# Performance work log

Hardware: AMD Instinct MI355X
Metric: run time of the kernel (lower is better)

Reference implementation:

```python
import jax, jax.numpy as jnp
import numpy as np

NUM_HEADS = 16
HEAD_DIM = 64
HIDDEN = NUM_HEADS * HEAD_DIM
LN_EPS = 1e-6


def setup_inputs() -> dict:
    key = jax.random.key(0)
    ks = jax.random.split(key, 5)
    B, T, H = 2, 2048, HIDDEN
    s = 1.0 / np.sqrt(H)
    return {
        "h": jax.random.normal(ks[0], (B, T, H), jnp.float32),
        "Wq": jax.random.normal(ks[1], (H, H), jnp.float32) * s,
        "bq": jnp.zeros((H,), jnp.float32),
        "Wk": jax.random.normal(ks[2], (H, H), jnp.float32) * s,
        "bk": jnp.zeros((H,), jnp.float32),
        "Wv": jax.random.normal(ks[3], (H, H), jnp.float32) * s,
        "bv": jnp.zeros((H,), jnp.float32),
        "Wo": jax.random.normal(ks[4], (H, H), jnp.float32) * s,
        "bo": jnp.zeros((H,), jnp.float32),
        "gamma": jnp.ones((H,), jnp.float32),
        "beta": jnp.zeros((H,), jnp.float32),
    }


def _split_heads(x):
    B, T, H = x.shape
    return x.reshape(B, T, NUM_HEADS, HEAD_DIM).transpose(0, 2, 1, 3)  # [B,h,T,d]


def reference(h, Wq, bq, Wk, bk, Wv, bv, Wo, bo, gamma, beta):
    # QKV projections (nn.Linear: x @ W^T + b)
    Q = _split_heads(h @ Wq.T + bq)
    K = _split_heads(h @ Wk.T + bk)
    V = _split_heads(h @ Wv.T + bv)
    scale = HEAD_DIM ** -0.5
    scores = jnp.einsum("bhqd,bhkd->bhqk", Q, K) * scale  # [B,h,T,T]
    attn = jax.nn.softmax(scores, axis=-1)
    ctx = jnp.einsum("bhqk,bhkd->bhqd", attn, V)          # [B,h,T,d]
    B, _, T, _ = ctx.shape
    ctx = ctx.transpose(0, 2, 1, 3).reshape(B, T, HIDDEN)
    out = ctx @ Wo.T + bo + h  # dropout is identity at eval
    # LayerNorm(eps=1e-6)
    mu = out.mean(-1, keepdims=True)
    var = jnp.mean((out - mu) ** 2, -1, keepdims=True)
    return (out - mu) * jax.lax.rsqrt(var + LN_EPS) * gamma + beta
```

## Files before the change

### kernel.cpp

```cpp
#include <hip/hip_runtime.h>
#include <hip/hip_bf16.h>

#define NH   16
#define HD   64
#define HID  1024
#define TSEQ 2048
#define BATCH 2
#define KSCALE 0.18033688011112042f

typedef __attribute__((ext_vector_type(4))) float f32x4;
typedef __attribute__((ext_vector_type(8))) short s16x8;
typedef __attribute__((ext_vector_type(4))) short s16x4;
typedef __attribute__((ext_vector_type(8))) _Float16 f16x8;
typedef __attribute__((ext_vector_type(4))) _Float16 f16x4;
typedef __attribute__((ext_vector_type(2))) _Float16 f16x2;

__device__ __forceinline__ unsigned short f2bf(float f) {
  union { float f; unsigned int u; } v; v.f = f;
  unsigned int r = v.u + 0x7fffu + ((v.u >> 16) & 1u);
  return (unsigned short)(r >> 16);
}
__device__ __forceinline__ float bf2f(unsigned short b) {
  union { unsigned int u; float f; } v; v.u = ((unsigned int)b) << 16; return v.f;
}

__device__ __forceinline__ void gll16(const void* g, void* l) {
  __builtin_amdgcn_global_load_lds(
      (const __attribute__((address_space(1))) unsigned int*)g,
      (__attribute__((address_space(3))) unsigned int*)l, 16, 0, 0);
}

#define WAITBAR(N)                                                      \
  do {                                                                  \
    __builtin_amdgcn_sched_barrier(0);                                  \
    asm volatile("s_waitcnt vmcnt(" #N ")\n\ts_barrier" ::: "memory");  \
  } while (0)

__global__ __launch_bounds__(256) void cast_all_k(
    const float* __restrict__ h,
    const float* __restrict__ w0, const float* __restrict__ w1,
    const float* __restrict__ w2, const float* __restrict__ w3,
    unsigned short* __restrict__ hb, unsigned short* __restrict__ wbase) {
  int i = blockIdx.x * 256 + threadIdx.x;
  const float* src; unsigned short* dst; int idx; float sc = 1.f;
  if (i < 1048576) { src = h; dst = hb; idx = i; }
  else {
    int idx4 = i - 1048576;
    int w = idx4 >> 18;
    idx = idx4 & 262143;
    src = (w == 0) ? w0 : (w == 1) ? w1 : (w == 2) ? w2 : w3;
    dst = wbase + (size_t)(idx4 - idx) * 4;
    if (w == 1) sc = KSCALE;
  }
  float4 v = ((const float4*)src)[idx];
  ushort4 o;
  o.x = f2bf(v.x * sc); o.y = f2bf(v.y * sc); o.z = f2bf(v.z * sc); o.w = f2bf(v.w * sc);
  ((ushort4*)dst)[idx] = o;
}

__global__ __launch_bounds__(256) void gemm_qkv(
    const unsigned short* __restrict__ hb,
    const unsigned short* __restrict__ wcat,
    const float* __restrict__ bq, const float* __restrict__ bk, const float* __restrict__ bv,
    unsigned short* __restrict__ qo, unsigned short* __restrict__ ko,
    unsigned short* __restrict__ vto) {
  __shared__ unsigned short Ash[4][128 * 32];
  __shared__ unsigned short Bsh[4][192 * 32];
  const int tid = threadIdx.x, lane = tid & 63, wave = tid >> 6;
  const int l15 = lane & 15, quad = lane >> 4;
  const int wr = wave >> 1, wc = wave & 1;
  const int bn = blockIdx.x * 192, bm = blockIdx.y * 128;
  const char* Ab = (const char*)(hb + (size_t)bm * HID);
  const char* Bb = (const char*)(wcat + (size_t)bn * HID);
  const int off = tid * 16;
  const int r0 = off >> 6, c0 = off & 63;
  const size_t ga0 = (size_t)r0 * (HID * 2) + c0;
  const size_t ga1 = ga0 + (size_t)64  * (HID * 2);
  const size_t gb2 = ga0 + (size_t)128 * (HID * 2);
  const int lb0 = wave * 512;
  const int lb1 = 2048 + wave * 512;
  const int lb2 = 4096 + wave * 512;

  f32x4 acc[4][6];
#pragma unroll
  for (int i = 0; i < 4; ++i)
#pragma unroll
    for (int j = 0; j < 6; ++j) acc[i][j] = f32x4{0.f, 0.f, 0.f, 0.f};

  auto stage = [&](int bufi, int k0) {
    const size_t kb = (size_t)k0 * 2;
    gll16(Ab + ga0 + kb, &Ash[bufi][lb0]);
    gll16(Ab + ga1 + kb, &Ash[bufi][lb1]);
    gll16(Bb + ga0 + kb, &Bsh[bufi][lb0]);
    gll16(Bb + ga1 + kb, &Bsh[bufi][lb1]);
    gll16(Bb + gb2 + kb, &Bsh[bufi][lb2]);
  };
  auto compute = [&](int bufi) {
    s16x8 af[4], bfr[6];
#pragma unroll
    for (int i = 0; i < 4; ++i)
      af[i] = *(const s16x8*)(&Ash[bufi][(wr * 64 + i * 16 + l15) * 32 + quad * 8]);
#pragma unroll
    for (int j = 0; j < 6; ++j)
      bfr[j] = *(const s16x8*)(&Bsh[bufi][(wc * 96 + j * 16 + l15) * 32 + quad * 8]);
#pragma unroll
    for (int i = 0; i < 4; ++i)
#pragma unroll
      for (int j = 0; j < 6; ++j)
        acc[i][j] = __builtin_amdgcn_mfma_f32_16x16x32_bf16(af[i], bfr[j], acc[i][j], 0, 0, 0);
  };

  stage(0, 0);
  stage(1, 32);
  stage(2, 64);
  int cur = 0, pf = 3;
  const int NT = HID / 32;
  for (int t = 0; t < NT - 3; ++t) {
    WAITBAR(10);
    stage(pf, (t + 3) * 32);
    compute(cur);
    cur = (cur + 1) & 3;
    pf  = (pf + 1) & 3;
  }
  WAITBAR(10); compute(cur); cur = (cur + 1) & 3;
  WAITBAR(5);  compute(cur); cur = (cur + 1) & 3;
  WAITBAR(0);  compute(cur);

  const int rbase = bm + wr * 64;
#pragma unroll
  for (int j = 0; j < 6; ++j) {
    const int cg  = bn + wc * 96 + j * 16;
    const int mat = cg >> 10;
    const int coln = (cg & 1023) + l15;
    const int head = coln >> 6, d = coln & 63;
    if (mat == 2) {
      const float bb = bv[coln];
#pragma unroll
      for (int i = 0; i < 4; ++i) {
        const int row0 = rbase + i * 16 + quad * 4;
        const int bI = row0 >> 11, t0 = row0 & 2047;
        unsigned short o[4];
#pragma unroll
        for (int r = 0; r < 4; ++r) {
          _Float16 hv = (_Float16)(acc[i][j][r] + bb);
          o[r] = __builtin_bit_cast(unsigned short, hv);
        }
        *(s16x4*)(vto + ((size_t)((bI * NH + head) * HD + d)) * TSEQ + t0) = *(const s16x4*)o;
      }
    } else {
      unsigned short* dst = (mat == 0) ? qo : ko;
      const float bb = (mat == 0) ? bq[coln] : bk[coln] * KSCALE;
#pragma unroll
      for (int i = 0; i < 4; ++i) {
#pragma unroll
        for (int r = 0; r < 4; ++r) {
          const int row = rbase + i * 16 + quad * 4 + r;
          const int bI = row >> 11, t = row & 2047;
          dst[(((size_t)(bI * NH + head) * TSEQ) + t) * HD + d] = f2bf(acc[i][j][r] + bb);
        }
      }
    }
  }
}

__global__ __launch_bounds__(256) void gemm_out(
    const unsigned short* __restrict__ ctx, const unsigned short* __restrict__ wo,
    const float* __restrict__ bo, const float* __restrict__ hres,
    float* __restrict__ outf) {
  __shared__ unsigned short Ash[5][128 * 32];
  __shared__ unsigned short Bsh[5][64 * 32];
  const int tid = threadIdx.x, lane = tid & 63, wave = tid >> 6;
  const int l15 = lane & 15, quad = lane >> 4;
  const int wr = wave >> 1, wc = wave & 1;
  const int bn = blockIdx.x * 64, bm = blockIdx.y * 128;
  const char* Ab = (const char*)(ctx + (size_t)bm * HID);
  const char* Bb = (const char*)(wo + (size_t)bn * HID);
  const int off = tid * 16;
  const int r0 = off >> 6, c0 = off & 63;
  const size_t ga0 = (size_t)r0 * (HID * 2) + c0;
  const size_t ga1 = ga0 + (size_t)64 * (HID * 2);
  const int lb0 = wave * 512, lb1 = 2048 + wave * 512;

  f32x4 acc[4][2];
#pragma unroll
  for (int i = 0; i < 4; ++i)
#pragma unroll
    for (int j = 0; j < 2; ++j) acc[i][j] = f32x4{0.f, 0.f, 0.f, 0.f};

  auto stage = [&](int bufi, int k0) {
    const size_t kb = (size_t)k0 * 2;
    gll16(Ab + ga0 + kb, &Ash[bufi][lb0]);
    gll16(Ab + ga1 + kb, &Ash[bufi][lb1]);
    gll16(Bb + ga0 + kb, &Bsh[bufi][lb0]);
  };
  auto compute = [&](int bufi) {
    s16x8 af[4], bfr[2];
#pragma unroll
    for (int i = 0; i < 4; ++i)
      af[i] = *(const s16x8*)(&Ash[bufi][(wr * 64 + i * 16 + l15) * 32 + quad * 8]);
#pragma unroll
    for (int j = 0; j < 2; ++j)
      bfr[j] = *(const s16x8*)(&Bsh[bufi][(wc * 32 + j * 16 + l15) * 32 + quad * 8]);
#pragma unroll
    for (int i = 0; i < 4; ++i)
#pragma unroll
      for (int j = 0; j < 2; ++j)
        acc[i][j] = __builtin_amdgcn_mfma_f32_16x16x32_bf16(af[i], bfr[j], acc[i][j], 0, 0, 0);
  };

  stage(0, 0);
  stage(1, 32);
  stage(2, 64);
  stage(3, 96);
  int cur = 0, pf = 4;
  const int NT = HID / 32;
  for (int t = 0; t < NT - 4; ++t) {
    WAITBAR(9);
    stage(pf, (t + 4) * 32);
    compute(cur);
    cur = (cur == 4) ? 0 : cur + 1;
    pf  = (pf  == 4) ? 0 : pf + 1;
  }
  WAITBAR(9); compute(cur); cur = (cur == 4) ? 0 : cur + 1;
  WAITBAR(6); compute(cur); cur = (cur == 4) ? 0 : cur + 1;
  WAITBAR(3); compute(cur); cur = (cur == 4) ? 0 : cur + 1;
  WAITBAR(0); compute(cur);

#pragma unroll
  for (int j = 0; j < 2; ++j) {
    const int col = bn + wc * 32 + j * 16 + l15;
    const float bb = bo[col];
#pragma unroll
    for (int i = 0; i < 4; ++i) {
#pragma unroll
      for (int r = 0; r < 4; ++r) {
        const int row = bm + wr * 64 + i * 16 + quad * 4 + r;
        const size_t o = (size_t)row * HID + col;
        outf[o] = acc[i][j][r] + bb + hres[o];
      }
    }
  }
}

__global__ __launch_bounds__(256, 2) void attn_k(
    const unsigned short* __restrict__ qb, const unsigned short* __restrict__ kb,
    const unsigned short* __restrict__ vt, unsigned short* __restrict__ ctx,
    unsigned short* __restrict__ Opart, float* __restrict__ rsumP,
    int lsplit, int ntiles) {
  __shared__ unsigned short Ksh[3][64 * 72];
  __shared__ unsigned short Vsh[3][64 * 72];

  const int tid = threadIdx.x, lane = tid & 63, wave = tid >> 6;
  const int l15 = lane & 15, quad = lane >> 4;
  const int z = blockIdx.z;
  const int b = z >> lsplit;
  const int part = z & ((1 << lsplit) - 1);
  const int h = blockIdx.y, qt = blockIdx.x;
  const size_t ho = ((size_t)(b * NH + h)) * TSEQ * HD;
  const unsigned short* Qh = qb + ho;
  const unsigned short* Kh = kb + ho;
  const unsigned short* Vh = vt + ho;
  const int q0 = qt * 128 + wave * 32;
  const int kt0 = part * ntiles;

  s16x8 qf[2][2];
#pragma unroll
  for (int s = 0; s < 2; ++s)
#pragma unroll
    for (int ks = 0; ks < 2; ++ks)
      qf[s][ks] = *(const s16x8*)(Qh + (size_t)(q0 + s * 16 + l15) * HD + ks * 32 + quad * 8);

  f32x4 accO[4][2];
  f32x4 accR[2];
#pragma unroll
  for (int n2 = 0; n2 < 4; ++n2)
#pragma unroll
    for (int s = 0; s < 2; ++s) accO[n2][s] = f32x4{0.f, 0.f, 0.f, 0.f};
  accR[0] = accR[1] = f32x4{0.f, 0.f, 0.f, 0.f};
  const f16x8 vones = {(_Float16)1.f, (_Float16)1.f, (_Float16)1.f, (_Float16)1.f,
                       (_Float16)1.f, (_Float16)1.f, (_Float16)1.f, (_Float16)1.f};

  const int sr = tid >> 3, sc = (tid & 7) * 8;
  const int c = tid & 7;
  const int vwb = (c >> 2) * 32 + (c & 1) * 16 + ((c & 3) >> 1) * 4;
  s16x8 kreg[2], vreg[2];

  auto ldregs = [&](int kt) {
    const int k0n = (kt0 + kt) * 64;
#pragma unroll
    for (int hf = 0; hf < 2; ++hf) {
      kreg[hf] = *(const s16x8*)(Kh + (size_t)(k0n + sr + hf * 32) * HD + sc);
      vreg[hf] = *(const s16x8*)(Vh + (size_t)(sr + hf * 32) * TSEQ + k0n + sc);
    }
  };
  auto wlds = [&](int bi) {
#pragma unroll
    for (int hf = 0; hf < 2; ++hf) {
      *(s16x8*)(Ksh[bi] + (sr + hf * 32) * 72 + sc) = kreg[hf];
      const s16x4* vh = (const s16x4*)&vreg[hf];
      *(s16x4*)(Vsh[bi] + (sr + hf * 32) * 72 + vwb)     = vh[0];
      *(s16x4*)(Vsh[bi] + (sr + hf * 32) * 72 + vwb + 8) = vh[1];
    }
  };

  f32x4 accS[2][4];
  f16x4 pP[2][4];

  auto qkt = [&](int bi) {
#pragma unroll
    for (int s = 0; s < 2; ++s)
#pragma unroll
      for (int n = 0; n < 4; ++n) accS[s][n] = f32x4{0.f, 0.f, 0.f, 0.f};
    __builtin_amdgcn_s_setprio(1);
#pragma unroll
    for (int ks = 0; ks < 2; ++ks) {
#pragma unroll
      for (int n = 0; n < 4; ++n) {
        s16x8 kf = *(const s16x8*)(Ksh[bi] + (n * 16 + l15) * 72 + ks * 32 + quad * 8);
#pragma unroll
        for (int s = 0; s < 2; ++s)
          accS[s][n] = __builtin_amdgcn_mfma_f32_16x16x32_bf16(kf, qf[s][ks], accS[s][n], 0, 0, 0);
      }
    }
    __builtin_amdgcn_s_setprio(0);
  };
  auto expp = [&]() {
#pragma unroll
    for (int s = 0; s < 2; ++s)
#pragma unroll
      for (int n = 0; n < 4; ++n) {
        float e0 = __builtin_amdgcn_exp2f(accS[s][n][0]);
        float e1 = __builtin_amdgcn_exp2f(accS[s][n][1]);
        float e2 = __builtin_amdgcn_exp2f(accS[s][n][2]);
        float e3 = __builtin_amdgcn_exp2f(accS[s][n][3]);
        f16x2 lo = __builtin_bit_cast(f16x2, __builtin_amdgcn_cvt_pkrtz(e0, e1));
        f16x2 hi = __builtin_bit_cast(f16x2, __builtin_amdgcn_cvt_pkrtz(e2, e3));
        pP[s][n] = f16x4{lo[0], lo[1], hi[0], hi[1]};
      }
  };
  auto pv = [&](int bi) {
    __builtin_amdgcn_s_setprio(1);
#pragma unroll
    for (int kk = 0; kk < 2; ++kk) {
      union { f16x4 h[2]; f16x8 v8; } u0, u1;
      u0.h[0] = pP[0][2 * kk]; u0.h[1] = pP[0][2 * kk + 1];
      u1.h[0] = pP[1][2 * kk]; u1.h[1] = pP[1][2 * kk + 1];
      accR[0] = __builtin_amdgcn_mfma_f32_16x16x32_f16(vones, u0.v8, accR[0], 0, 0, 0);
      accR[1] = __builtin_amdgcn_mfma_f32_16x16x32_f16(vones, u1.v8, accR[1], 0, 0, 0);
#pragma unroll
      for (int n2 = 0; n2 < 4; ++n2) {
        f16x8 vA = *(const f16x8*)(Vsh[bi] + (n2 * 16 + l15) * 72 + kk * 32 + quad * 8);
        accO[n2][0] = __builtin_amdgcn_mfma_f32_16x16x32_f16(vA, u0.v8, accO[n2][0], 0, 0, 0);
        accO[n2][1] = __builtin_amdgcn_mfma_f32_16x16x32_f16(vA, u1.v8, accO[n2][1], 0, 0, 0);
      }
    }
    __builtin_amdgcn_s_setprio(0);
  };

  ldregs(0);
  wlds(0);
  __syncthreads();
  if (ntiles > 1) ldregs(1);
  qkt(0);
  expp();

  int b0 = 0, b1 = 1;
  for (int t = 0; t < ntiles - 1; ++t) {
    wlds(b1);
    __syncthreads();
    if (t + 2 < ntiles) ldregs(t + 2);
    qkt(b1);
    pv(b0);
    expp();
    b0 = b1; b1 = (b1 == 2) ? 0 : b1 + 1;
  }
  pv(b0);

  float rsum[2] = {accR[0][0], accR[1][0]};

  if (lsplit) {
    const int slot = (part * BATCH + b) * NH + h;
    const size_t ob = (size_t)slot * TSEQ * HD;
#pragma unroll
    for (int s = 0; s < 2; ++s) {
      const int t = q0 + s * 16 + l15;
#pragma unroll
      for (int n2 = 0; n2 < 4; ++n2) {
        const int d0 = n2 * 16 + quad * 4;
        unsigned short o[4];
#pragma unroll
        for (int r = 0; r < 4; ++r) o[r] = f2bf(accO[n2][s][r]);
        *(s16x4*)(Opart + ob + (size_t)t * HD + d0) = *(const s16x4*)o;
      }
    }
    if (quad == 0) {
      const size_t rb = (size_t)slot * TSEQ;
#pragma unroll
      for (int s = 0; s < 2; ++s)
        rsumP[rb + q0 + s * 16 + l15] = rsum[s];
    }
  } else {
#pragma unroll
    for (int s = 0; s < 2; ++s) {
      const int t = q0 + s * 16 + l15;
      const float inv = 1.f / rsum[s];
#pragma unroll
      for (int n2 = 0; n2 < 4; ++n2) {
        const int d0 = n2 * 16 + quad * 4;
        unsigned short o[4];
#pragma unroll
        for (int r = 0; r < 4; ++r) o[r] = f2bf(accO[n2][s][r] * inv);
        *(s16x4*)(ctx + ((size_t)(b * TSEQ + t)) * HID + h * HD + d0) = *(const s16x4*)o;
      }
    }
  }
}

__global__ __launch_bounds__(256) void combine_k(
    const unsigned short* __restrict__ Opart, const float* __restrict__ rsumP,
    unsigned short* __restrict__ ctx, int nparts) {
  const int gtid = blockIdx.x * 256 + threadIdx.x;
  const int d = (gtid & 7) * 8;
  const int rem = gtid >> 3;
  const int t = rem & 2047;
  const int bh = rem >> 11;
  float acc[8] = {0, 0, 0, 0, 0, 0, 0, 0};
  float rs = 0.f;
  for (int p = 0; p < nparts; ++p) {
    const int slot = p * 32 + bh;
    s16x8 a = *(const s16x8*)(Opart + ((size_t)slot * TSEQ + t) * HD + d);
#pragma unroll
    for (int j = 0; j < 8; ++j) acc[j] += bf2f(((const unsigned short*)&a)[j]);
    rs += rsumP[(size_t)slot * TSEQ + t];
  }
  const float inv = 1.f / rs;
  unsigned short o[8];
#pragma unroll
  for (int j = 0; j < 8; ++j) o[j] = f2bf(acc[j] * inv);
  const int b = bh >> 4, h = bh & 15;
  *(s16x8*)(ctx + ((size_t)(b * TSEQ + t)) * HID + h * HD + d) = *(const s16x8*)o;
}

__global__ __launch_bounds__(256) void ln_k(float* __restrict__ io,
                                            const float* __restrict__ gamma,
                                            const float* __restrict__ beta) {
  const int row = blockIdx.x, tid = threadIdx.x;
  float x[4]; float s = 0.f, s2 = 0.f;
#pragma unroll
  for (int i = 0; i < 4; ++i) {
    x[i] = io[(size_t)row * HID + tid + i * 256];
    s += x[i]; s2 += x[i] * x[i];
  }
#pragma unroll
  for (int off = 1; off < 64; off <<= 1) {
    s  += __shfl_xor(s, off, 64);
    s2 += __shfl_xor(s2, off, 64);
  }
  __shared__ float red[8];
  const int wave = tid >> 6;
  if ((tid & 63) == 0) { red[wave] = s; red[wave + 4] = s2; }
  __syncthreads();
  s  = red[0] + red[1] + red[2] + red[3];
  s2 = red[4] + red[5] + red[6] + red[7];
  const float mean = s * (1.f / HID);
  const float var  = s2 * (1.f / HID) - mean * mean;
  const float rstd = rsqrtf(var + 1e-6f);
#pragma unroll
  for (int i = 0; i < 4; ++i) {
    const int col = tid + i * 256;
    io[(size_t)row * HID + col] = (x[i] - mean) * rstd * gamma[col] + beta[col];
  }
}

extern "C" void kernel_launch(void* const* d_in, const int* in_sizes, int n_in,
                              void* d_out, int out_size, void* d_ws, size_t ws_size,
                              hipStream_t stream) {
  const float* h    = (const float*)d_in[0];
  const float* Wq   = (const float*)d_in[1];
  const float* bq   = (const float*)d_in[2];
  const float* Wk   = (const float*)d_in[3];
  const float* bk   = (const float*)d_in[4];
  const float* Wv   = (const float*)d_in[5];
  const float* bv   = (const float*)d_in[6];
  const float* Wo   = (const float*)d_in[7];
  const float* bo   = (const float*)d_in[8];
  const float* gamma = (const float*)d_in[9];
  const float* beta  = (const float*)d_in[10];
  float* out = (float*)d_out;

  unsigned short* hb   = (unsigned short*)d_ws;
  unsigned short* wqb  = hb  + 4194304;
  unsigned short* wkb  = wqb + 1048576;
  unsigned short* wvb  = wkb + 1048576;
  unsigned short* wob  = wvb + 1048576;
  unsigned short* qb   = wob + 1048576;
  unsigned short* kb   = qb  + 4194304;
  unsigned short* vtf  = kb  + 4194304;
  unsigned short* Opart = vtf + 4194304;
  unsigned short* ctxb = hb;
  float* rsumP = (float*)(Opart + 4194304);

  cast_all_k<<<8192, 256, 0, stream>>>(h, Wq, Wk, Wv, Wo, hb, wqb);
  gemm_qkv<<<dim3(16, 32), 256, 0, stream>>>(hb, wqb, bq, bk, bv, qb, kb, vtf);
  attn_k<<<dim3(TSEQ / 128, NH, BATCH), 256, 0, stream>>>(
      qb, kb, vtf, ctxb, Opart, rsumP, 0, 32);
  gemm_out<<<dim3(16, 32), 256, 0, stream>>>(ctxb, wob, bo, h, out);
  ln_k<<<4096, 256, 0, stream>>>(out, gamma, beta);
}
```

Before: 198.4 us.

## Restructure QKV GEMM into 256x192 tiles with 512 threads and swizzled double-buffered LDS

Rewrites the QKV projection GEMM to use 8 waves per block over a 256x192 output tile with BK=64. The old 4-stage BK=32 ring is replaced by a double-buffered pipeline split into four phases, with prefetch of the next tile interleaved between them. LDS rows are XOR-swizzled to avoid bank conflicts, and s_setprio is raised around the MFMA bursts. The larger tile improves operand reuse and cuts the block count, but it adds barriers per k-step and needs more LDS (about 112KB), which limits occupancy. The unused combine kernel is also removed.

```diff
diff --git a/kernel.cpp b/kernel.cpp
--- a/kernel.cpp
+++ b/kernel.cpp
@@ -58,85 +58,124 @@
   ((ushort4*)dst)[idx] = o;
 }
 
-__global__ __launch_bounds__(256) void gemm_qkv(
+__global__ __launch_bounds__(512) void gemm_qkv(
     const unsigned short* __restrict__ hb,
     const unsigned short* __restrict__ wcat,
     const float* __restrict__ bq, const float* __restrict__ bk, const float* __restrict__ bv,
     unsigned short* __restrict__ qo, unsigned short* __restrict__ ko,
     unsigned short* __restrict__ vto) {
-  __shared__ unsigned short Ash[4][128 * 32];
-  __shared__ unsigned short Bsh[4][192 * 32];
+  __shared__ unsigned short Alds[2][256 * 64];
+  __shared__ unsigned short Blds[2][192 * 64];
   const int tid = threadIdx.x, lane = tid & 63, wave = tid >> 6;
   const int l15 = lane & 15, quad = lane >> 4;
-  const int wr = wave >> 1, wc = wave & 1;
-  const int bn = blockIdx.x * 192, bm = blockIdx.y * 128;
+  const int wr = wave >> 2, wc = wave & 3;
+  const int bn = blockIdx.x * 192, bm = blockIdx.y * 256;
   const char* Ab = (const char*)(hb + (size_t)bm * HID);
   const char* Bb = (const char*)(wcat + (size_t)bn * HID);
-  const int off = tid * 16;
-  const int r0 = off >> 6, c0 = off & 63;
-  const size_t ga0 = (size_t)r0 * (HID * 2) + c0;
-  const size_t ga1 = ga0 + (size_t)64  * (HID * 2);
-  const size_t gb2 = ga0 + (size_t)128 * (HID * 2);
-  const int lb0 = wave * 512;
-  const int lb1 = 2048 + wave * 512;
-  const int lb2 = 4096 + wave * 512;
-
-  f32x4 acc[4][6];
-#pragma unroll
-  for (int i = 0; i < 4; ++i)
-#pragma unroll
-    for (int j = 0; j < 6; ++j) acc[i][j] = f32x4{0.f, 0.f, 0.f, 0.f};
-
-  auto stage = [&](int bufi, int k0) {
-    const size_t kb = (size_t)k0 * 2;
-    gll16(Ab + ga0 + kb, &Ash[bufi][lb0]);
-    gll16(Ab + ga1 + kb, &Ash[bufi][lb1]);
-    gll16(Bb + ga0 + kb, &Bsh[bufi][lb0]);
-    gll16(Bb + ga1 + kb, &Bsh[bufi][lb1]);
-    gll16(Bb + gb2 + kb, &Bsh[bufi][lb2]);
-  };
-  auto compute = [&](int bufi) {
-    s16x8 af[4], bfr[6];
-#pragma unroll
-    for (int i = 0; i < 4; ++i)
-      af[i] = *(const s16x8*)(&Ash[bufi][(wr * 64 + i * 16 + l15) * 32 + quad * 8]);
-#pragma unroll
-    for (int j = 0; j < 6; ++j)
-      bfr[j] = *(const s16x8*)(&Bsh[bufi][(wc * 96 + j * 16 + l15) * 32 + quad * 8]);
-#pragma unroll
-    for (int i = 0; i < 4; ++i)
-#pragma unroll
-      for (int j = 0; j < 6; ++j)
-        acc[i][j] = __builtin_amdgcn_mfma_f32_16x16x32_bf16(af[i], bfr[j], acc[i][j], 0, 0, 0);
-  };
-
-  stage(0, 0);
-  stage(1, 32);
-  stage(2, 64);
-  int cur = 0, pf = 3;
-  const int NT = HID / 32;
-  for (int t = 0; t < NT - 3; ++t) {
-    WAITBAR(10);
-    stage(pf, (t + 3) * 32);
-    compute(cur);
-    cur = (cur + 1) & 3;
-    pf  = (pf + 1) & 3;
-  }
-  WAITBAR(10); compute(cur); cur = (cur + 1) & 3;
-  WAITBAR(5);  compute(cur); cur = (cur + 1) & 3;
-  WAITBAR(0);  compute(cur);
-
-  const int rbase = bm + wr * 64;
-#pragma unroll
-  for (int j = 0; j < 6; ++j) {
-    const int cg  = bn + wc * 96 + j * 16;
+  const int srow = tid >> 3;
+  const int csw = ((tid & 7) ^ (srow & 7)) * 16;
+  const size_t arow = (size_t)srow * (HID * 2) + csw;
+  const int ldst = wave * 1024;
+
+  f32x4 acc[8][3];
+#pragma unroll
+  for (int i = 0; i < 8; ++i)
+#pragma unroll
+    for (int j = 0; j < 3; ++j) acc[i][j] = f32x4{0.f, 0.f, 0.f, 0.f};
+
+  auto stageA = [&](int tt) {
+    const int s = tt & 1;
+    const size_t kb = (size_t)tt * 128;
+    char* Ad = (char*)&Alds[s][0];
+#pragma unroll
+    for (int n = 0; n < 4; ++n)
+      gll16(Ab + (size_t)(n * 64) * (HID * 2) + arow + kb, Ad + n * 8192 + ldst);
+  };
+  auto stageB = [&](int tt) {
+    const int s = tt & 1;
+    const size_t kb = (size_t)tt * 128;
+    char* Bd = (char*)&Blds[s][0];
+#pragma unroll
+    for (int m = 0; m < 3; ++m)
+      gll16(Bb + (size_t)(m * 64) * (HID * 2) + arow + kb, Bd + m * 8192 + ldst);
+  };
+
+  s16x8 afr[2][2], bfr[3][2];
+  auto rdB = [&](int s) {
+#pragma unroll
+    for (int j = 0; j < 3; ++j)
+#pragma unroll
+      for (int kk = 0; kk < 2; ++kk) {
+        const int row = wc * 48 + j * 16 + l15;
+        const int byt = row * 128 + (((kk * 4 + quad) ^ (row & 7)) * 16);
+        bfr[j][kk] = *(const s16x8*)((const char*)&Blds[s][0] + byt);
+      }
+  };
+  auto rdA = [&](int s, int p) {
+#pragma unroll
+    for (int di = 0; di < 2; ++di)
+#pragma unroll
+      for (int kk = 0; kk < 2; ++kk) {
+        const int row = wr * 128 + (2 * p + di) * 16 + l15;
+        const int byt = row * 128 + (((kk * 4 + quad) ^ (row & 7)) * 16);
+        afr[di][kk] = *(const s16x8*)((const char*)&Alds[s][0] + byt);
+      }
+  };
+  auto mm = [&](int p) {
+    __builtin_amdgcn_s_setprio(1);
+#pragma unroll
+    for (int di = 0; di < 2; ++di)
+#pragma unroll
+      for (int j = 0; j < 3; ++j)
+#pragma unroll
+        for (int kk = 0; kk < 2; ++kk)
+          acc[2 * p + di][j] =
+              __builtin_amdgcn_mfma_f32_16x16x32_bf16(afr[di][kk], bfr[j][kk],
+                                                      acc[2 * p + di][j], 0, 0, 0);
+    __builtin_amdgcn_s_setprio(0);
+  };
+
+#define PHASE_MID                                          \
+  __builtin_amdgcn_s_barrier();                            \
+  asm volatile("s_waitcnt lgkmcnt(0)" ::: "memory");       \
+  __builtin_amdgcn_sched_barrier(0);
+
+  stageA(0); stageB(0);
+  asm volatile("s_waitcnt vmcnt(0)" ::: "memory");
+  __builtin_amdgcn_s_barrier();
+
+  const int NT = HID / 64;
+  for (int t = 0; t < NT; ++t) {
+    const int s = t & 1;
+    rdA(s, 0); rdB(s);
+    if (t + 1 < NT) stageA(t + 1);
+    PHASE_MID; mm(0);
+    __builtin_amdgcn_s_barrier();
+    rdA(s, 1);
+    if (t + 1 < NT) stageB(t + 1);
+    PHASE_MID; mm(1);
+    __builtin_amdgcn_s_barrier();
+    rdA(s, 2);
+    PHASE_MID; mm(2);
+    __builtin_amdgcn_s_barrier();
+    rdA(s, 3);
+    asm volatile("s_waitcnt vmcnt(0)" ::: "memory");
+    PHASE_MID; mm(3);
+    __builtin_amdgcn_s_barrier();
+  }
+#undef PHASE_MID
+
+  const int rbase = bm + wr * 128;
+#pragma unroll
+  for (int j = 0; j < 3; ++j) {
+    const int cg  = bn + wc * 48 + j * 16;
     const int mat = cg >> 10;
     const int coln = (cg & 1023) + l15;
     const int head = coln >> 6, d = coln & 63;
     if (mat == 2) {
       const float bb = bv[coln];
 #pragma unroll
-      for (int i = 0; i < 4; ++i) {
+      for (int i = 0; i < 8; ++i) {
         const int row0 = rbase + i * 16 + quad * 4;
         const int bI = row0 >> 11, t0 = row0 & 2047;
         unsigned short o[4];
@@ -151,7 +190,7 @@
       unsigned short* dst = (mat == 0) ? qo : ko;
       const float bb = (mat == 0) ? bq[coln] : bk[coln] * KSCALE;
 #pragma unroll
-      for (int i = 0; i < 4; ++i) {
+      for (int i = 0; i < 8; ++i) {
 #pragma unroll
         for (int r = 0; r < 4; ++r) {
           const int row = rbase + i * 16 + quad * 4 + r;
@@ -416,31 +455,6 @@
   }
 }
 
-__global__ __launch_bounds__(256) void combine_k(
-    const unsigned short* __restrict__ Opart, const float* __restrict__ rsumP,
-    unsigned short* __restrict__ ctx, int nparts) {
-  const int gtid = blockIdx.x * 256 + threadIdx.x;
-  const int d = (gtid & 7) * 8;
-  const int rem = gtid >> 3;
-  const int t = rem & 2047;
-  const int bh = rem >> 11;
-  float acc[8] = {0, 0, 0, 0, 0, 0, 0, 0};
-  float rs = 0.f;
-  for (int p = 0; p < nparts; ++p) {
-    const int slot = p * 32 + bh;
-    s16x8 a = *(const s16x8*)(Opart + ((size_t)slot * TSEQ + t) * HD + d);
-#pragma unroll
-    for (int j = 0; j < 8; ++j) acc[j] += bf2f(((const unsigned short*)&a)[j]);
-    rs += rsumP[(size_t)slot * TSEQ + t];
-  }
-  const float inv = 1.f / rs;
-  unsigned short o[8];
-#pragma unroll
-  for (int j = 0; j < 8; ++j) o[j] = f2bf(acc[j] * inv);
-  const int b = bh >> 4, h = bh & 15;
-  *(s16x8*)(ctx + ((size_t)(b * TSEQ + t)) * HID + h * HD + d) = *(const s16x8*)o;
-}
-
 __global__ __launch_bounds__(256) void ln_k(float* __restrict__ io,
                                             const float* __restrict__ gamma,
                                             const float* __restrict__ beta) {
@@ -501,7 +515,7 @@
   float* rsumP = (float*)(Opart + 4194304);
 
   cast_all_k<<<8192, 256, 0, stream>>>(h, Wq, Wk, Wv, Wo, hb, wqb);
-  gemm_qkv<<<dim3(16, 32), 256, 0, stream>>>(hb, wqb, bq, bk, bv, qb, kb, vtf);
+  gemm_qkv<<<dim3(16, 16), 512, 0, stream>>>(hb, wqb, bq, bk, bv, qb, kb, vtf);
   attn_k<<<dim3(TSEQ / 128, NH, BATCH), 256, 0, stream>>>(
       qb, kb, vtf, ctxb, Opart, rsumP, 0, 32);
   gemm_out<<<dim3(16, 32), 256, 0, stream>>>(ctxb, wob, bo, h, out);
```

After: 202.4 us. 2.0% more time.
